# Performance work log

Measured on AMD Instinct MI355X. Metric: run time of the kernel, lower is better.

## Reference

```python
import jax, jax.numpy as jnp
import numpy as np

B, S = 8, 1024
DM = 512            # d_model arg
D = 2 * DM          # actual feature width (1024)
H = 16
DK = D // H         # 64
DV = 2 * 32         # per-head value dim (2*d_v) = 64
DI = 2048           # d_inner
K = 4               # d_conv, dilation 2 -> effective 7, pad 3 each side
EPS = 1e-6


def setup_inputs() -> dict:
    key = jax.random.key(0)
    ks = jax.random.split(key, 16)
    s = lambda k, shape, fan: jax.random.normal(k, shape, jnp.float32) / np.sqrt(fan)
    return {
        "x": jax.random.normal(ks[0], (B, S, D), jnp.float32),
        "mask": jnp.ones((B, 1, 1, S), jnp.int32),
        "gamma": jnp.ones((D,), jnp.float32),
        "wq": s(ks[1], (D, H * DK), D),
        "wk": s(ks[2], (D, H * DK), D),
        "wv": s(ks[3], (D, H * DV), D),
        "wo": s(ks[4], (H * DV, D), H * DV),
        "w1": s(ks[5], (DM, DI), DM),
        "b1": jnp.zeros((DI,), jnp.float32),
        "cw": s(ks[6], (DI, 1, K), K),   # depthwise conv kernel [O, I/groups=1, K]
        "cb": jnp.zeros((DI,), jnp.float32),
        "w2": s(ks[7], (DM, DI), DM),
        "b2": jnp.zeros((DI,), jnp.float32),
        "wp": s(ks[8], (DI, D), DI),
        "bp": jnp.zeros((D,), jnp.float32),
    }


def reference(x, mask, gamma, wq, wk, wv, wo, w1, b1, cw, cb, w2, b2, wp, bp):
    # RMSNorm
    nrm = x * jax.lax.rsqrt(jnp.mean(x * x, axis=-1, keepdims=True) + EPS) * gamma
    # Multi-head attention
    q = (nrm @ wq).reshape(B, S, H, DK).transpose(0, 2, 1, 3)
    k = (nrm @ wk).reshape(B, S, H, DK).transpose(0, 2, 1, 3)
    v = (nrm @ wv).reshape(B, S, H, DV).transpose(0, 2, 1, 3)
    scores = jnp.einsum('bhqd,bhkd->bhqk', q, k) / np.sqrt(DK).astype(np.float32)
    scores = jnp.where(mask == 0, jnp.float32(-1e9), scores)
    attn = jax.nn.softmax(scores, axis=-1)
    ctx = jnp.einsum('bhqk,bhkd->bhqd', attn, v)        # [B,H,S,DV]
    ctx = ctx.transpose(0, 2, 1, 3).reshape(B, S, H * DV)
    out = ctx @ wo                                       # [B,S,D]
    # split into two halves
    f_in, s_in = out[:, :, :D // 2], out[:, :, D // 2:]
    # FirstSection: linear -> depthwise dilated conv (padding 'same')
    f = f_in @ w1 + b1                                   # [B,S,DI]
    f = f.transpose(0, 2, 1)                             # [B,DI,S]
    f = jax.lax.conv_general_dilated(
        f, cw, window_strides=(1,), padding=[(3, 3)], rhs_dilation=(2,),
        feature_group_count=DI, dimension_numbers=('NCH', 'OIH', 'NCH'))
    f = (f + cb[None, :, None]).transpose(0, 2, 1)       # [B,S,DI]
    # SecondSection: linear + relu
    sec = jax.nn.relu(s_in @ w2 + b2)                    # [B,S,DI]
    gated = f * sec
    return x + (gated @ wp + bp)
```

## Files before the change

### kernel.cpp

```cpp
#include <hip/hip_runtime.h>

typedef unsigned short u16;
typedef __bf16 bf16x8 __attribute__((ext_vector_type(8)));
typedef short  s16x8  __attribute__((ext_vector_type(8)));
typedef float  f32x4  __attribute__((ext_vector_type(4)));

#define LDSPAD 72

#define GLOAD16(gp, lp) __builtin_amdgcn_global_load_lds( \
  (__attribute__((address_space(1))) unsigned int*)(unsigned long long)(const void*)(gp), \
  (__attribute__((address_space(3))) unsigned int*)(lp), 16, 0, 0)

static __device__ __forceinline__ u16 f2bf(float f){
  union { float f; unsigned int u; } v; v.f = f;
  unsigned int r = v.u + 0x7fffu + ((v.u >> 16) & 1u);
  return (u16)(r >> 16);
}
static __device__ __forceinline__ float bf2f(u16 u){
  union { unsigned int u; float f; } v; v.u = ((unsigned int)u) << 16; return v.f;
}
static __device__ __forceinline__ unsigned fbits(float f){
  union { float f; unsigned u; } v; v.f = f; return v.u;
}

__global__ __launch_bounds__(256) void wtrans4_kernel(
    const float* __restrict__ in0, const float* __restrict__ in1,
    const float* __restrict__ in2, const float* __restrict__ in3,
    u16* __restrict__ out0, u16* __restrict__ out1,
    u16* __restrict__ out2, u16* __restrict__ out3, int K, int N){
  __shared__ float tile[32][33];
  int z = blockIdx.z;
  const float* in = (z == 0) ? in0 : (z == 1) ? in1 : (z == 2) ? in2 : in3;
  u16* out = (z == 0) ? out0 : (z == 1) ? out1 : (z == 2) ? out2 : out3;
  int n0 = blockIdx.x * 32, k0 = blockIdx.y * 32;
  int tx = threadIdx.x, ty = threadIdx.y;
  #pragma unroll
  for (int i = 0; i < 4; ++i)
    tile[ty + i*8][tx] = in[(size_t)(k0 + ty + i*8) * N + n0 + tx];
  __syncthreads();
  #pragma unroll
  for (int i = 0; i < 4; ++i)
    out[(size_t)(n0 + ty + i*8) * K + k0 + tx] = f2bf(tile[tx][ty + i*8]);
}

__global__ __launch_bounds__(256) void cwtrans_kernel(const float* __restrict__ cw,
                                                      float* __restrict__ cwT){
  int i = blockIdx.x * 256 + threadIdx.x;
  int c = i >> 2, j = i & 3;
  cwT[j * 2048 + c] = cw[i];
}

__global__ __launch_bounds__(256) void rmsnorm_kernel(const float* __restrict__ x,
                                                      const float* __restrict__ gamma,
                                                      u16* __restrict__ out){
  int row = blockIdx.x;
  const float* xr = x + (size_t)row * 1024;
  int tid = threadIdx.x;
  float4 xv = *(const float4*)(xr + tid * 4);
  float ss = xv.x*xv.x + xv.y*xv.y + xv.z*xv.z + xv.w*xv.w;
  #pragma unroll
  for (int off = 1; off < 64; off <<= 1) ss += __shfl_xor(ss, off);
  __shared__ float wsum[4];
  if ((tid & 63) == 0) wsum[tid >> 6] = ss;
  __syncthreads();
  float tot = wsum[0] + wsum[1] + wsum[2] + wsum[3];
  float r = rsqrtf(tot * (1.0f/1024.0f) + 1e-6f);
  const float4 gv = *(const float4*)(gamma + tid * 4);
  u16* o = out + (size_t)row * 1024 + tid * 4;
  o[0] = f2bf(xv.x * r * gv.x);
  o[1] = f2bf(xv.y * r * gv.y);
  o[2] = f2bf(xv.z * r * gv.z);
  o[3] = f2bf(xv.w * r * gv.w);
}

template<int EPI>
__global__ __launch_bounds__(256) void gemm128_kernel(
    const u16* __restrict__ A, int lda,
    const u16* __restrict__ Bt,
    const float* __restrict__ bias,
    const float* __restrict__ b2x,
    u16* __restrict__ outb, float* __restrict__ outf,
    u16* __restrict__ vt,
    int N, int K, float scale, int nm)
{
  __shared__ __align__(16) u16 Sh[2*128*64];
  u16* As = Sh;
  u16* Bs = Sh + 128*64;
  int tid = threadIdx.x;
  int wid = tid >> 6, lane = tid & 63;
  int fr = lane & 15, fq = lane >> 4;
  int wr = wid >> 1, wc = wid & 1;
  int l = (int)blockIdx.x;
  int m0 = (l % nm) * 128, n0 = (l / nm) * 128;
  int srow = lane >> 3;
  int csw  = (lane & 7) ^ srow;
  int c7   = fr & 7;
  f32x4 acc[4][4] = {};

  const u16* Abase = A + ((EPI == 6 && n0 >= 2048) ? 512 : 0) + (size_t)m0 * lda;
  const u16* Bbase = Bt + (size_t)n0 * K;

  auto STAGE = [&](int kt){
    int k0 = kt << 6;
    #pragma unroll
    for (int i = 0; i < 4; ++i){
      int r = i*32 + wid*8;
      GLOAD16(Abase + (size_t)(r + srow) * lda + k0 + csw*8, &As[r*64]);
      GLOAD16(Bbase + (size_t)(r + srow) * K   + k0 + csw*8, &Bs[r*64]);
    }
  };

  int nt = K >> 6;
  for (int kt = 0; kt < nt; ++kt){
    if (kt) __syncthreads();
    STAGE(kt);
    __syncthreads();
    #pragma unroll
    for (int ks = 0; ks < 2; ++ks){
      bf16x8 av[4], bv[4];
      #pragma unroll
      for (int mi = 0; mi < 4; ++mi)
        av[mi] = *(const bf16x8*)&As[(wr*64 + mi*16 + fr)*64 + (((ks*4 + fq) ^ c7) * 8)];
      #pragma unroll
      for (int ni = 0; ni < 4; ++ni)
        bv[ni] = *(const bf16x8*)&Bs[(wc*64 + ni*16 + fr)*64 + (((ks*4 + fq) ^ c7) * 8)];
      #pragma unroll
      for (int mi = 0; mi < 4; ++mi)
        #pragma unroll
        for (int ni = 0; ni < 4; ++ni)
          acc[mi][ni] = __builtin_amdgcn_mfma_f32_16x16x32_bf16(av[mi], bv[ni], acc[mi][ni], 0, 0, 0);
    }
  }

  if (EPI == 5 && n0 >= 2048){
    u16* Ct = Sh;
    #pragma unroll
    for (int p = 0; p < 2; ++p){
      __syncthreads();
      if (wc == p){
        #pragma unroll
        for (int ni = 0; ni < 4; ++ni)
          #pragma unroll
          for (int mi = 0; mi < 4; ++mi){
            int cl = ni*16 + fr;
            int rl = wr*64 + mi*16 + fq*4;
            uint2 pk;
            pk.x = (unsigned)f2bf(acc[mi][ni][0]) | ((unsigned)f2bf(acc[mi][ni][1]) << 16);
            pk.y = (unsigned)f2bf(acc[mi][ni][2]) | ((unsigned)f2bf(acc[mi][ni][3]) << 16);
            *(uint2*)&Ct[cl*136 + rl] = pk;
          }
      }
      __syncthreads();
      #pragma unroll
      for (int ci = 0; ci < 4; ++ci){
        int qq = ci*256 + tid;
        int c = qq >> 4, off = (qq & 15) * 8;
        uint4 v = *(const uint4*)&Ct[c*136 + off];
        *(uint4*)&vt[(size_t)(n0 - 2048 + p*64 + c) * 8192 + m0 + off] = v;
      }
    }
    return;
  }

  #pragma unroll
  for (int ni = 0; ni < 4; ++ni){
    int col = n0 + wc*64 + ni*16 + fr;
    bool fp = (EPI != 6) || (col < 2048);
    int cc  = (EPI == 6) ? (col & 2047) : col;
    float bvv = 0.0f;
    if (EPI == 3) bvv = bias[col];
    if (EPI == 6) bvv = fp ? bias[cc] : b2x[cc];
    float scl = (EPI == 5) ? ((col < 1024) ? scale : 1.0f) : scale;
    #pragma unroll
    for (int mi = 0; mi < 4; ++mi){
      #pragma unroll
      for (int j = 0; j < 4; ++j){
        int row = m0 + wr*64 + mi*16 + fq*4 + j;
        float vv = acc[mi][ni][j] * scl + bvv;
        size_t idx = (size_t)row * N + cc;
        if (EPI == 3)      outf[idx] = vv + b2x[idx];
        else if (EPI == 6){
          if (!fp) vv = fmaxf(vv, 0.0f);
          (fp ? outb : vt)[idx] = f2bf(vv);
        } else             outb[idx] = f2bf(vv);
      }
    }
  }
}

__global__ __launch_bounds__(256) void attn_kernel(
    const u16* __restrict__ qkv, const u16* __restrict__ Vt,
    const int* __restrict__ mask, u16* __restrict__ ctx)
{
  __shared__ __align__(16) u16 Ks[64*64];
  __shared__ __align__(16) u16 Vs[64*64];
  __shared__ __align__(16) u16 Ps[64][LDSPAD];
  int tid = threadIdx.x;
  int wid = tid >> 6, lane = tid & 63;
  int fr = lane & 15, fq = lane >> 4;
  int i = (int)blockIdx.x;
  int wg = (i & 7) * 256 + (i >> 3);
  int bh = wg >> 4;
  int q0 = (wg & 15) * 64;
  int b = bh >> 4, h = bh & 15;

  const u16* qb  = qkv + (size_t)b * 1024 * 3072 + h * 64;
  const u16* kb  = qb + 1024;
  const u16* vtb = Vt + (size_t)(h * 64) * 8192 + b * 1024;

  int lrow = lane >> 3;
  int cs   = (lane & 7) ^ lrow;
  int wbase = wid * 16;
  int c7 = fr & 7;

  bf16x8 qf[2];
  {
    const u16* qp = qb + (size_t)(q0 + wid*16 + fr) * 3072 + fq * 8;
    qf[0] = *(const bf16x8*)(qp);
    qf[1] = *(const bf16x8*)(qp + 32);
  }
  f32x4 acc[4];
  #pragma unroll
  for (int k = 0; k < 4; ++k) acc[k] = (f32x4){0.f, 0.f, 0.f, 0.f};
  float mrun = -1e30f, lsum = 0.f;

  auto STAGE = [&](int t){
    int kv0 = t * 64;
    #pragma unroll
    for (int k = 0; k < 2; ++k){
      int r = wbase + k*8 + lrow;
      GLOAD16(kb  + (size_t)(kv0 + r) * 3072 + cs * 8, &Ks[(wbase + k*8) * 64]);
      GLOAD16(vtb + (size_t)r * 8192 + kv0 + cs * 8,   &Vs[(wbase + k*8) * 64]);
    }
  };

  STAGE(0);
  for (int t = 0; t < 16; ++t){
    int kv0 = t * 64;
    __syncthreads();
    bf16x8 kf[2][4], vf[2][4];
    #pragma unroll
    for (int ks = 0; ks < 2; ++ks)
      #pragma unroll
      for (int nt = 0; nt < 4; ++nt){
        kf[ks][nt] = *(const bf16x8*)&Ks[(nt*16 + fr)*64 + (((ks*4 + fq) ^ c7) * 8)];
        vf[ks][nt] = *(const bf16x8*)&Vs[(nt*16 + fr)*64 + (((ks*4 + fq) ^ c7) * 8)];
      }
    int mv1 = mask[b * 1024 + kv0 + lane];
    __syncthreads();
    if (t + 1 < 16) STAGE(t + 1);

    f32x4 sc[4];
    #pragma unroll
    for (int nt = 0; nt < 4; ++nt) sc[nt] = (f32x4){0.f, 0.f, 0.f, 0.f};
    __builtin_amdgcn_s_setprio(1);
    #pragma unroll
    for (int ks = 0; ks < 2; ++ks)
      #pragma unroll
      for (int nt = 0; nt < 4; ++nt)
        sc[nt] = __builtin_amdgcn_mfma_f32_16x16x32_bf16(kf[ks][nt], qf[ks], sc[nt], 0, 0, 0);
    __builtin_amdgcn_s_setprio(0);

    if (!__all(mv1 != 0)){
      #pragma unroll
      for (int nt = 0; nt < 4; ++nt){
        int4 mv = *(const int4*)&mask[b * 1024 + kv0 + nt*16 + fq*4];
        int mvals[4] = {mv.x, mv.y, mv.z, mv.w};
        #pragma unroll
        for (int j = 0; j < 4; ++j)
          sc[nt][j] = mvals[j] ? sc[nt][j] : -1e9f;
      }
    }

    float m01 = fmaxf(fmaxf(sc[0][0], sc[0][1]), fmaxf(sc[0][2], sc[0][3]));
    float m11 = fmaxf(fmaxf(sc[1][0], sc[1][1]), fmaxf(sc[1][2], sc[1][3]));
    float m21 = fmaxf(fmaxf(sc[2][0], sc[2][1]), fmaxf(sc[2][2], sc[2][3]));
    float m31 = fmaxf(fmaxf(sc[3][0], sc[3][1]), fmaxf(sc[3][2], sc[3][3]));
    float pmax = fmaxf(fmaxf(m01, m11), fmaxf(m21, m31));
    pmax = fmaxf(pmax, __shfl_xor(pmax, 16));
    pmax = fmaxf(pmax, __shfl_xor(pmax, 32));
    if (!__all(pmax <= mrun + 8.0f)){
      float mnew = fmaxf(mrun, pmax);
      float corr = exp2f(mrun - mnew);
      #pragma unroll
      for (int nt = 0; nt < 4; ++nt)
        #pragma unroll
        for (int j = 0; j < 4; ++j)
          acc[nt][j] *= corr;
      lsum *= corr;
      mrun = mnew;
    }
    float p[4][4];
    float ls = 0.f;
    #pragma unroll
    for (int nt = 0; nt < 4; ++nt)
      #pragma unroll
      for (int j = 0; j < 4; ++j){
        float pv = exp2f(sc[nt][j] - mrun);
        p[nt][j] = pv;
        ls += pv;
      }
    lsum += ls;

    #pragma unroll
    for (int nt = 0; nt < 4; ++nt){
      unsigned d0 = __builtin_amdgcn_perm(fbits(p[nt][1]), fbits(p[nt][0]), 0x07060302u);
      unsigned d1 = __builtin_amdgcn_perm(fbits(p[nt][3]), fbits(p[nt][2]), 0x07060302u);
      *(unsigned*)&Ps[wid*16 + fr][nt*16 + fq*4]     = d0;
      *(unsigned*)&Ps[wid*16 + fr][nt*16 + fq*4 + 2] = d1;
    }

    __builtin_amdgcn_s_setprio(1);
    #pragma unroll
    for (int ks = 0; ks < 2; ++ks){
      bf16x8 pb = *(const bf16x8*)&Ps[wid*16 + fr][ks*32 + fq*8];
      #pragma unroll
      for (int nt = 0; nt < 4; ++nt)
        acc[nt] = __builtin_amdgcn_mfma_f32_16x16x32_bf16(vf[ks][nt], pb, acc[nt], 0, 0, 0);
    }
    __builtin_amdgcn_s_setprio(0);
  }

  lsum += __shfl_xor(lsum, 16);
  lsum += __shfl_xor(lsum, 32);
  float invl = 1.0f / lsum;

  size_t rowbase = ((size_t)b * 1024 + q0 + wid*16 + fr) * 1024 + h * 64;
  #pragma unroll
  for (int nt = 0; nt < 4; ++nt){
    unsigned lo = (unsigned)f2bf(acc[nt][0] * invl) | ((unsigned)f2bf(acc[nt][1] * invl) << 16);
    unsigned hi = (unsigned)f2bf(acc[nt][2] * invl) | ((unsigned)f2bf(acc[nt][3] * invl) << 16);
    uint2 pk; pk.x = lo; pk.y = hi;
    *(uint2*)&ctx[rowbase + nt*16 + fq*4] = pk;
  }
}

__global__ __launch_bounds__(256) void convgate_kernel(
    const u16* __restrict__ f, const float* __restrict__ cwT,
    const float* __restrict__ cb, u16* __restrict__ sec_inout)
{
  size_t gid = (size_t)blockIdx.x * blockDim.x + threadIdx.x;
  int c0 = (int)(gid & 255) * 8;
  int t  = (int)((gid >> 8) & 1023);
  int b  = (int)(gid >> 18);
  const u16* fb = f + ((size_t)b * 1024) * 2048;

  float4 w[4][2];
  #pragma unroll
  for (int j = 0; j < 4; ++j){
    w[j][0] = *(const float4*)&cwT[j*2048 + c0];
    w[j][1] = *(const float4*)&cwT[j*2048 + c0 + 4];
  }
  float4 cb0 = *(const float4*)&cb[c0];
  float4 cb1 = *(const float4*)&cb[c0 + 4];
  float acc[8] = {cb0.x, cb0.y, cb0.z, cb0.w, cb1.x, cb1.y, cb1.z, cb1.w};

  #pragma unroll
  for (int j = 0; j < 4; ++j){
    int tt = t - 3 + 2 * j;
    if (tt >= 0 && tt < 1024){
      s16x8 fv = *(const s16x8*)(fb + (size_t)tt * 2048 + c0);
      const float* wj = (const float*)&w[j][0];
      #pragma unroll
      for (int e = 0; e < 8; ++e) acc[e] += bf2f((u16)fv[e]) * wj[e];
    }
  }
  u16* sp = sec_inout + (((size_t)b * 1024 + t) * 2048 + c0);
  s16x8 sv = *(const s16x8*)sp;
  s16x8 ov;
  #pragma unroll
  for (int e = 0; e < 8; ++e) ov[e] = (short)f2bf(acc[e] * bf2f((u16)sv[e]));
  *(s16x8*)sp = ov;
}

extern "C" void kernel_launch(void* const* d_in, const int* in_sizes, int n_in,
                              void* d_out, int out_size, void* d_ws, size_t ws_size,
                              hipStream_t stream)
{
  const float* x     = (const float*)d_in[0];
  const int*   mask  = (const int*)  d_in[1];
  const float* gamma = (const float*)d_in[2];
  const float* wq    = (const float*)d_in[3];
  const float* wk    = (const float*)d_in[4];
  const float* wv    = (const float*)d_in[5];
  const float* wo    = (const float*)d_in[6];
  const float* w1    = (const float*)d_in[7];
  const float* b1    = (const float*)d_in[8];
  const float* cw    = (const float*)d_in[9];
  const float* cb    = (const float*)d_in[10];
  const float* w2    = (const float*)d_in[11];
  const float* b2    = (const float*)d_in[12];
  const float* wp    = (const float*)d_in[13];
  const float* bp    = (const float*)d_in[14];
  float* out = (float*)d_out;

  char* p = (char*)d_ws;
  auto alloc = [&](size_t bytes){ char* r = p; p += (bytes + 255) & ~(size_t)255; return r; };
  u16*   wqkvT = (u16*)alloc((size_t)3072*1024*2);
  u16*   woT   = (u16*)alloc((size_t)1024*1024*2);
  u16*   w12T  = (u16*)alloc((size_t)4096*512*2);
  u16*   wpT   = (u16*)alloc((size_t)1024*2048*2);
  float* cwT   = (float*)alloc((size_t)4*2048*4);
  u16*   nrm   = (u16*)alloc((size_t)8192*1024*2);
  u16*   qkv   = (u16*)alloc((size_t)8192*3072*2);
  u16*   sec   = (u16*)alloc((size_t)8192*2048*2);
  u16* Vt   = sec;
  u16* ao   = qkv;
  u16* fbuf = qkv + (size_t)8192*1024;
  (void)ws_size; (void)in_sizes; (void)n_in; (void)out_size;

  const float QSCALE = 0.125f * 1.44269504088896340736f;

  dim3 tb32(32, 8);
  wtrans4_kernel<<<dim3(32, 32, 4), tb32, 0, stream>>>(
      wq, wk, wv, wo,
      wqkvT, wqkvT + (size_t)1024*1024, wqkvT + (size_t)2048*1024, woT, 1024, 1024);
  wtrans4_kernel<<<dim3(64, 16, 2), tb32, 0, stream>>>(
      w1, w2, w1, w2, w12T, w12T + (size_t)2048*512, w12T, w12T + (size_t)2048*512, 512, 2048);
  wtrans4_kernel<<<dim3(32, 64, 1), tb32, 0, stream>>>(
      wp, wp, wp, wp, wpT, wpT, wpT, wpT, 2048, 1024);
  cwtrans_kernel<<<32, 256, 0, stream>>>(cw, cwT);

  rmsnorm_kernel<<<8192, 256, 0, stream>>>(x, gamma, nrm);

  gemm128_kernel<5><<<1536, 256, 0, stream>>>(nrm, 1024, wqkvT, nullptr, nullptr, qkv, nullptr, Vt, 3072, 1024, QSCALE, 64);

  attn_kernel<<<2048, 256, 0, stream>>>(qkv, Vt, mask, nrm);

  gemm128_kernel<0><<<512, 256, 0, stream>>>(nrm, 1024, woT, nullptr, nullptr, ao, nullptr, nullptr, 1024, 1024, 1.0f, 64);

  gemm128_kernel<6><<<2048, 256, 0, stream>>>(ao, 1024, w12T, b1, b2, fbuf, nullptr, sec, 2048, 512, 1.0f, 64);

  convgate_kernel<<<8192, 256, 0, stream>>>(fbuf, cwT, cb, sec);

  gemm128_kernel<3><<<512, 256, 0, stream>>>(sec, 2048, wpT, bp, x, nullptr, out, nullptr, 1024, 2048, 1.0f, 64);
}
```

Measured before the change: 312.3 us.

## Switch GEMMs to 256x256 tiles with double-buffered LDS and 8 waves

Replaces the 128x128 single-buffered GEMM with a 256x256 tile kernel using 512 threads, a 32-wide K step, double-buffered LDS staging that prefetches the next tile while computing the current one, and s_setprio around MFMA bursts. The V-transpose epilogue now writes packed columns directly to global memory instead of transposing through LDS. Larger tiles raise arithmetic intensity and halve barriers per MFMA, but the grid shrinks to 128 blocks for some GEMMs, which can underfill the 256 CUs, and the direct V stores are narrower and less coalesced.

New measurement: 371.5 us. +18.9%, slower.

```diff
diff --git a/kernel.cpp b/kernel.cpp
--- a/kernel.cpp
+++ b/kernel.cpp
@@ -74,7 +74,7 @@
 }
 
 template<int EPI>
-__global__ __launch_bounds__(256) void gemm128_kernel(
+__global__ __launch_bounds__(512, 2) void gemm256_kernel(
     const u16* __restrict__ A, int lda,
     const u16* __restrict__ Bt,
     const float* __restrict__ bias,
@@ -83,88 +83,61 @@
     u16* __restrict__ vt,
     int N, int K, float scale, int nm)
 {
-  __shared__ __align__(16) u16 Sh[2*128*64];
-  u16* As = Sh;
-  u16* Bs = Sh + 128*64;
+  __shared__ __align__(16) u16 As[2][256*32];
+  __shared__ __align__(16) u16 Bs[2][256*32];
   int tid = threadIdx.x;
-  int wid = tid >> 6, lane = tid & 63;
+  int w = tid >> 6, lane = tid & 63;
   int fr = lane & 15, fq = lane >> 4;
-  int wr = wid >> 1, wc = wid & 1;
+  int wm = w >> 2, wn = w & 3;
   int l = (int)blockIdx.x;
-  int m0 = (l % nm) * 128, n0 = (l / nm) * 128;
-  int srow = lane >> 3;
-  int csw  = (lane & 7) ^ srow;
-  int c7   = fr & 7;
-  f32x4 acc[4][4] = {};
+  int m0 = (l % nm) * 256, n0 = (l / nm) * 256;
+  int ch = (fq + ((fr >> 1) & 3)) & 3;
+  int sr = lane >> 2;
+  int cg = ((lane & 3) - ((lane >> 3) & 3)) & 3;
+  f32x4 acc[8][4] = {};
 
   const u16* Abase = A + ((EPI == 6 && n0 >= 2048) ? 512 : 0) + (size_t)m0 * lda;
   const u16* Bbase = Bt + (size_t)n0 * K;
 
-  auto STAGE = [&](int kt){
-    int k0 = kt << 6;
-    #pragma unroll
-    for (int i = 0; i < 4; ++i){
-      int r = i*32 + wid*8;
-      GLOAD16(Abase + (size_t)(r + srow) * lda + k0 + csw*8, &As[r*64]);
-      GLOAD16(Bbase + (size_t)(r + srow) * K   + k0 + csw*8, &Bs[r*64]);
+  auto STAGE = [&](int bsel, int kt){
+    int k0 = kt << 5;
+    #pragma unroll
+    for (int g = 0; g < 2; ++g){
+      int r = g*128 + w*16 + sr;
+      GLOAD16(Abase + (size_t)r * lda + k0 + cg*8, &As[bsel][(g*128 + w*16)*32]);
+      GLOAD16(Bbase + (size_t)r * K   + k0 + cg*8, &Bs[bsel][(g*128 + w*16)*32]);
     }
   };
 
-  int nt = K >> 6;
-  for (int kt = 0; kt < nt; ++kt){
-    if (kt) __syncthreads();
-    STAGE(kt);
+  int ntk = K >> 5;
+  STAGE(0, 0);
+  __syncthreads();
+  for (int kt = 0; kt < ntk; ++kt){
+    int cur = kt & 1;
+    if (kt + 1 < ntk) STAGE(cur ^ 1, kt + 1);
+    bf16x8 bfr[4];
+    #pragma unroll
+    for (int ni = 0; ni < 4; ++ni)
+      bfr[ni] = *(const bf16x8*)&Bs[cur][(wn*64 + ni*16 + fr)*32 + ch*8];
+    #pragma unroll
+    for (int q = 0; q < 4; ++q){
+      bf16x8 a0 = *(const bf16x8*)&As[cur][(wm*128 + (2*q)*16   + fr)*32 + ch*8];
+      bf16x8 a1 = *(const bf16x8*)&As[cur][(wm*128 + (2*q+1)*16 + fr)*32 + ch*8];
+      __builtin_amdgcn_s_setprio(1);
+      #pragma unroll
+      for (int ni = 0; ni < 4; ++ni)
+        acc[2*q][ni]   = __builtin_amdgcn_mfma_f32_16x16x32_bf16(a0, bfr[ni], acc[2*q][ni], 0, 0, 0);
+      #pragma unroll
+      for (int ni = 0; ni < 4; ++ni)
+        acc[2*q+1][ni] = __builtin_amdgcn_mfma_f32_16x16x32_bf16(a1, bfr[ni], acc[2*q+1][ni], 0, 0, 0);
+      __builtin_amdgcn_s_setprio(0);
+    }
     __syncthreads();
-    #pragma unroll
-    for (int ks = 0; ks < 2; ++ks){
-      bf16x8 av[4], bv[4];
-      #pragma unroll
-      for (int mi = 0; mi < 4; ++mi)
-        av[mi] = *(const bf16x8*)&As[(wr*64 + mi*16 + fr)*64 + (((ks*4 + fq) ^ c7) * 8)];
-      #pragma unroll
-      for (int ni = 0; ni < 4; ++ni)
-        bv[ni] = *(const bf16x8*)&Bs[(wc*64 + ni*16 + fr)*64 + (((ks*4 + fq) ^ c7) * 8)];
-      #pragma unroll
-      for (int mi = 0; mi < 4; ++mi)
-        #pragma unroll
-        for (int ni = 0; ni < 4; ++ni)
-          acc[mi][ni] = __builtin_amdgcn_mfma_f32_16x16x32_bf16(av[mi], bv[ni], acc[mi][ni], 0, 0, 0);
-    }
-  }
-
-  if (EPI == 5 && n0 >= 2048){
-    u16* Ct = Sh;
-    #pragma unroll
-    for (int p = 0; p < 2; ++p){
-      __syncthreads();
-      if (wc == p){
-        #pragma unroll
-        for (int ni = 0; ni < 4; ++ni)
-          #pragma unroll
-          for (int mi = 0; mi < 4; ++mi){
-            int cl = ni*16 + fr;
-            int rl = wr*64 + mi*16 + fq*4;
-            uint2 pk;
-            pk.x = (unsigned)f2bf(acc[mi][ni][0]) | ((unsigned)f2bf(acc[mi][ni][1]) << 16);
-            pk.y = (unsigned)f2bf(acc[mi][ni][2]) | ((unsigned)f2bf(acc[mi][ni][3]) << 16);
-            *(uint2*)&Ct[cl*136 + rl] = pk;
-          }
-      }
-      __syncthreads();
-      #pragma unroll
-      for (int ci = 0; ci < 4; ++ci){
-        int qq = ci*256 + tid;
-        int c = qq >> 4, off = (qq & 15) * 8;
-        uint4 v = *(const uint4*)&Ct[c*136 + off];
-        *(uint4*)&vt[(size_t)(n0 - 2048 + p*64 + c) * 8192 + m0 + off] = v;
-      }
-    }
-    return;
   }
 
   #pragma unroll
   for (int ni = 0; ni < 4; ++ni){
-    int col = n0 + wc*64 + ni*16 + fr;
+    int col = n0 + wn*64 + ni*16 + fr;
     bool fp = (EPI != 6) || (col < 2048);
     int cc  = (EPI == 6) ? (col & 2047) : col;
     float bvv = 0.0f;
@@ -172,17 +145,25 @@
     if (EPI == 6) bvv = fp ? bias[cc] : b2x[cc];
     float scl = (EPI == 5) ? ((col < 1024) ? scale : 1.0f) : scale;
     #pragma unroll
-    for (int mi = 0; mi < 4; ++mi){
-      #pragma unroll
-      for (int j = 0; j < 4; ++j){
-        int row = m0 + wr*64 + mi*16 + fq*4 + j;
-        float vv = acc[mi][ni][j] * scl + bvv;
-        size_t idx = (size_t)row * N + cc;
-        if (EPI == 3)      outf[idx] = vv + b2x[idx];
-        else if (EPI == 6){
-          if (!fp) vv = fmaxf(vv, 0.0f);
-          (fp ? outb : vt)[idx] = f2bf(vv);
-        } else             outb[idx] = f2bf(vv);
+    for (int mi = 0; mi < 8; ++mi){
+      if (EPI == 5 && col >= 2048){
+        int row0 = m0 + wm*128 + mi*16 + fq*4;
+        uint2 pk;
+        pk.x = (unsigned)f2bf(acc[mi][ni][0]) | ((unsigned)f2bf(acc[mi][ni][1]) << 16);
+        pk.y = (unsigned)f2bf(acc[mi][ni][2]) | ((unsigned)f2bf(acc[mi][ni][3]) << 16);
+        *(uint2*)&vt[(size_t)(col - 2048) * 8192 + row0] = pk;
+      } else {
+        #pragma unroll
+        for (int j = 0; j < 4; ++j){
+          int row = m0 + wm*128 + mi*16 + fq*4 + j;
+          float vv = acc[mi][ni][j] * scl + bvv;
+          size_t idx = (size_t)row * N + cc;
+          if (EPI == 3)      outf[idx] = vv + b2x[idx];
+          else if (EPI == 6){
+            if (!fp) vv = fmaxf(vv, 0.0f);
+            (fp ? outb : vt)[idx] = f2bf(vv);
+          } else             outb[idx] = f2bf(vv);
+        }
       }
     }
   }
@@ -423,15 +404,15 @@
 
   rmsnorm_kernel<<<8192, 256, 0, stream>>>(x, gamma, nrm);
 
-  gemm128_kernel<5><<<1536, 256, 0, stream>>>(nrm, 1024, wqkvT, nullptr, nullptr, qkv, nullptr, Vt, 3072, 1024, QSCALE, 64);
+  gemm256_kernel<5><<<384, 512, 0, stream>>>(nrm, 1024, wqkvT, nullptr, nullptr, qkv, nullptr, Vt, 3072, 1024, QSCALE, 32);
 
   attn_kernel<<<2048, 256, 0, stream>>>(qkv, Vt, mask, nrm);
 
-  gemm128_kernel<0><<<512, 256, 0, stream>>>(nrm, 1024, woT, nullptr, nullptr, ao, nullptr, nullptr, 1024, 1024, 1.0f, 64);
-
-  gemm128_kernel<6><<<2048, 256, 0, stream>>>(ao, 1024, w12T, b1, b2, fbuf, nullptr, sec, 2048, 512, 1.0f, 64);
+  gemm256_kernel<0><<<128, 512, 0, stream>>>(nrm, 1024, woT, nullptr, nullptr, ao, nullptr, nullptr, 1024, 1024, 1.0f, 32);
+
+  gemm256_kernel<6><<<512, 512, 0, stream>>>(ao, 1024, w12T, b1, b2, fbuf, nullptr, sec, 2048, 512, 1.0f, 32);
 
   convgate_kernel<<<8192, 256, 0, stream>>>(fbuf, cwT, cb, sec);
 
-  gemm128_kernel<3><<<512, 256, 0, stream>>>(sec, 2048, wpT, bp, x, nullptr, out, nullptr, 1024, 2048, 1.0f, 64);
-}
+  gemm256_kernel<3><<<128, 512, 0, stream>>>(sec, 2048, wpT, bp, x, nullptr, out, nullptr, 1024, 2048, 1.0f, 32);
+}
```

## Triple-buffer GEMM K-tiles with async LDS prefetch two steps ahead

Applied to the files above, without the earlier changes.

The 128x128 bf16 GEMM main loop drops the single 64-wide K tile that was loaded and then consumed behind two barriers per iteration. It now uses three LDS buffers of 32-wide K tiles, prefetching tile kt+2 through global_load_lds while tile kt is fed to MFMA. There is one barrier per step, with vmcnt waits to track outstanding loads and s_setprio raised around the MFMA block. The goal is to hide global-memory latency behind compute and cut barrier stalls. The cost is twice as many loop iterations, a new swizzle for the narrower tile, and more LDS in use.

Measured after the change: 314.3 us. No clear change (+0.6%).

```diff
diff --git a/kernel.cpp b/kernel.cpp
--- a/kernel.cpp
+++ b/kernel.cpp
@@ -83,57 +83,64 @@
     u16* __restrict__ vt,
     int N, int K, float scale, int nm)
 {
-  __shared__ __align__(16) u16 Sh[2*128*64];
-  u16* As = Sh;
-  u16* Bs = Sh + 128*64;
+  __shared__ __align__(16) u16 As[3][128*32];
+  __shared__ __align__(16) u16 Bs[3][128*32];
   int tid = threadIdx.x;
   int wid = tid >> 6, lane = tid & 63;
   int fr = lane & 15, fq = lane >> 4;
   int wr = wid >> 1, wc = wid & 1;
   int l = (int)blockIdx.x;
   int m0 = (l % nm) * 128, n0 = (l / nm) * 128;
-  int srow = lane >> 3;
-  int csw  = (lane & 7) ^ srow;
-  int c7   = fr & 7;
+  int rl  = tid >> 2;
+  int cg  = (lane & 3) ^ ((lane >> 2) & 3);
+  int crd = (fq ^ (fr & 3)) * 8;
   f32x4 acc[4][4] = {};
 
   const u16* Abase = A + ((EPI == 6 && n0 >= 2048) ? 512 : 0) + (size_t)m0 * lda;
   const u16* Bbase = Bt + (size_t)n0 * K;
 
-  auto STAGE = [&](int kt){
-    int k0 = kt << 6;
-    #pragma unroll
-    for (int i = 0; i < 4; ++i){
-      int r = i*32 + wid*8;
-      GLOAD16(Abase + (size_t)(r + srow) * lda + k0 + csw*8, &As[r*64]);
-      GLOAD16(Bbase + (size_t)(r + srow) * K   + k0 + csw*8, &Bs[r*64]);
+  auto STAGE = [&](int bsel, int kt){
+    int k0 = kt << 5;
+    #pragma unroll
+    for (int i = 0; i < 2; ++i){
+      GLOAD16(Abase + (size_t)(i*64 + rl) * lda + k0 + cg*8, &As[bsel][(i*64 + wid*16)*32]);
+      GLOAD16(Bbase + (size_t)(i*64 + rl) * K   + k0 + cg*8, &Bs[bsel][(i*64 + wid*16)*32]);
     }
   };
 
-  int nt = K >> 6;
-  for (int kt = 0; kt < nt; ++kt){
-    if (kt) __syncthreads();
-    STAGE(kt);
-    __syncthreads();
-    #pragma unroll
-    for (int ks = 0; ks < 2; ++ks){
-      bf16x8 av[4], bv[4];
-      #pragma unroll
-      for (int mi = 0; mi < 4; ++mi)
-        av[mi] = *(const bf16x8*)&As[(wr*64 + mi*16 + fr)*64 + (((ks*4 + fq) ^ c7) * 8)];
+  int ntk = K >> 5;
+  STAGE(0, 0);
+  STAGE(1, 1);
+  asm volatile("s_waitcnt vmcnt(4)" ::: "memory");
+  __builtin_amdgcn_s_barrier();
+  for (int kt = 0; kt < ntk; ++kt){
+    int cur = kt % 3;
+    bf16x8 av[4], bv[4];
+    #pragma unroll
+    for (int mi = 0; mi < 4; ++mi)
+      av[mi] = *(const bf16x8*)&As[cur][(wr*64 + mi*16 + fr)*32 + crd];
+    #pragma unroll
+    for (int ni = 0; ni < 4; ++ni)
+      bv[ni] = *(const bf16x8*)&Bs[cur][(wc*64 + ni*16 + fr)*32 + crd];
+    if (kt + 2 < ntk) STAGE((kt + 2) % 3, kt + 2);
+    asm volatile("s_waitcnt lgkmcnt(0)" ::: "memory");
+    __builtin_amdgcn_sched_barrier(0);
+    __builtin_amdgcn_s_setprio(1);
+    #pragma unroll
+    for (int mi = 0; mi < 4; ++mi)
       #pragma unroll
       for (int ni = 0; ni < 4; ++ni)
-        bv[ni] = *(const bf16x8*)&Bs[(wc*64 + ni*16 + fr)*64 + (((ks*4 + fq) ^ c7) * 8)];
-      #pragma unroll
-      for (int mi = 0; mi < 4; ++mi)
-        #pragma unroll
-        for (int ni = 0; ni < 4; ++ni)
-          acc[mi][ni] = __builtin_amdgcn_mfma_f32_16x16x32_bf16(av[mi], bv[ni], acc[mi][ni], 0, 0, 0);
+        acc[mi][ni] = __builtin_amdgcn_mfma_f32_16x16x32_bf16(av[mi], bv[ni], acc[mi][ni], 0, 0, 0);
+    __builtin_amdgcn_s_setprio(0);
+    if (kt + 1 < ntk){
+      if (kt + 2 < ntk) asm volatile("s_waitcnt vmcnt(4)" ::: "memory");
+      else              asm volatile("s_waitcnt vmcnt(0)" ::: "memory");
+      __builtin_amdgcn_s_barrier();
     }
   }
 
   if (EPI == 5 && n0 >= 2048){
-    u16* Ct = Sh;
+    u16* Ct = &As[0][0];
     #pragma unroll
     for (int p = 0; p < 2; ++p){
       __syncthreads();
@@ -143,11 +150,11 @@
           #pragma unroll
           for (int mi = 0; mi < 4; ++mi){
             int cl = ni*16 + fr;
-            int rl = wr*64 + mi*16 + fq*4;
+            int rl2 = wr*64 + mi*16 + fq*4;
             uint2 pk;
             pk.x = (unsigned)f2bf(acc[mi][ni][0]) | ((unsigned)f2bf(acc[mi][ni][1]) << 16);
             pk.y = (unsigned)f2bf(acc[mi][ni][2]) | ((unsigned)f2bf(acc[mi][ni][3]) << 16);
-            *(uint2*)&Ct[cl*136 + rl] = pk;
+            *(uint2*)&Ct[cl*136 + rl2] = pk;
           }
       }
       __syncthreads();
```
